# Optimization experiments

Hardware: AMD Instinct MI355X
Metric: run time of the kernel (lower is better)

The kernel has to match this reference:

```python
import jax, jax.numpy as jnp
import numpy as np

HEADS = 4
DIM_HEAD = 32
SCALE = DIM_HEAD ** (-0.5)


def setup_inputs() -> dict:
    key = jax.random.key(0)
    k1, k2, k3, k4 = jax.random.split(key, 4)
    dim = 256
    hidden = HEADS * DIM_HEAD  # 128
    x = jax.random.normal(k1, (8, dim, 48, 48), dtype=jnp.float32)
    w_qkv = jax.random.normal(k2, (3 * hidden, dim), dtype=jnp.float32) * (dim ** -0.5)
    w_out = jax.random.normal(k3, (dim, hidden), dtype=jnp.float32) * (hidden ** -0.5)
    b_out = jax.random.normal(k4, (dim,), dtype=jnp.float32) * 0.01
    return {"x": x, "w_qkv": w_qkv, "w_out": w_out, "b_out": b_out}


def reference(x, w_qkv, w_out, b_out):
    b, c, h, w = x.shape
    n = h * w
    xf = x.reshape(b, c, n)                                  # [b, c, n]
    # 1x1 Conv1d (no bias) == pointwise linear over channels
    qkv = jnp.einsum('oc,bcn->bon', w_qkv, xf)               # [b, 3*hidden, n]
    q, k, v = jnp.split(qkv, 3, axis=1)                      # each [b, hidden, n]
    def to_heads(t):
        return t.reshape(b, HEADS, DIM_HEAD, n)              # b h d n
    q, k, v = to_heads(q) * SCALE, to_heads(k), to_heads(v)
    sim = jnp.einsum('bhdi,bhdj->bhij', q, k)                # [b, h, n, n]
    attn = jax.nn.softmax(sim, axis=-1)                      # stable (max-subtracted)
    out = jnp.einsum('bhij,bhdj->bhid', attn, v)             # [b, h, n, d]
    # 'b h (x y) d -> b (h d) x y'
    out = out.transpose(0, 1, 3, 2).reshape(b, HEADS * DIM_HEAD, n)
    y = jnp.einsum('oc,bcn->bon', w_out, out) + b_out[None, :, None]
    return y.reshape(b, c, h, w)
```

## Files before the change

kernel.cpp:

```cpp
#include <hip/hip_runtime.h>
#include <math.h>

#define NB    8
#define CDIM  256
#define NN    2304
#define NH    4
#define DH    32
#define HIDC  128
#define OC3   384
#define SCALE_LOG2E 0.25503524964550864f
#define SEG   2359296
#define LSEG  73728
#define PPARTS 4
#define JCHUNK 576
#define NITER  18

typedef short  bf16x8 __attribute__((ext_vector_type(8)));
typedef float  f32x4  __attribute__((ext_vector_type(4)));

__device__ __forceinline__ unsigned short f2bf(float f) {
    union { float f; unsigned u; } a; a.f = f;
    unsigned r = a.u + 0x7fffu + ((a.u >> 16) & 1u);
    return (unsigned short)(r >> 16);
}

__device__ __forceinline__ unsigned pack_trunc(float lo, float hi) {
    union { float f; unsigned u; } a, b; a.f = lo; b.f = hi;
    return (b.u & 0xFFFF0000u) | (a.u >> 16);
}

__device__ __forceinline__ float bflo(unsigned u) {
    union { unsigned u; float f; } c; c.u = u << 16; return c.f;
}
__device__ __forceinline__ float bfhi(unsigned u) {
    union { unsigned u; float f; } c; c.u = u & 0xFFFF0000u; return c.f;
}

__global__ __launch_bounds__(256) void qkv_proj_kernel(
    const float* __restrict__ x, const float* __restrict__ w,
    unsigned short* __restrict__ qt, unsigned short* __restrict__ kt,
    unsigned short* __restrict__ vtT)
{
    __shared__ unsigned short As[128 * 40];
    __shared__ unsigned short Bs[128 * 40];
    const int Lb   = (int)blockIdx.x;
    const int xcd  = Lb & 7;
    const int t    = Lb >> 3;
    const int sel  = t % 3;
    const int gl   = t / 3;
    const int group = gl * 8 + xcd;
    const int nb   = group % 18;
    const int b    = group / 18;
    const int n0 = nb * 128;
    const int o0 = sel * 128;

    const int tid  = (int)threadIdx.x;
    const int wave = tid >> 6;
    const int lane = tid & 63;
    const int li   = lane & 15;
    const int g    = lane >> 4;
    const int wm = (wave & 1) * 64;
    const int wn = (wave >> 1) * 64;
    const float* xb = x + (size_t)b * CDIM * NN;

    const int aco = (tid & 7) * 4;
    const int aor = tid >> 3;
    const int n4  = (tid & 31) * 4;
    const int c4  = (tid >> 5) * 4;

    f32x4 acc[4][4];
#pragma unroll
    for (int i = 0; i < 4; ++i)
#pragma unroll
        for (int j = 0; j < 4; ++j) acc[i][j] = (f32x4){0.f, 0.f, 0.f, 0.f};

    float4 wv[4], xv[4];
#pragma unroll
    for (int r = 0; r < 4; ++r)
        wv[r] = *(const float4*)&w[(size_t)(o0 + aor + 32 * r) * CDIM + aco];
#pragma unroll
    for (int dd = 0; dd < 4; ++dd)
        xv[dd] = *(const float4*)&xb[(size_t)(c4 + dd) * NN + n0 + n4];

    for (int k0 = 0; k0 < CDIM; k0 += 32) {
        __syncthreads();
#pragma unroll
        for (int r = 0; r < 4; ++r) {
            uint2 pk;
            pk.x = (unsigned)f2bf(wv[r].x) | ((unsigned)f2bf(wv[r].y) << 16);
            pk.y = (unsigned)f2bf(wv[r].z) | ((unsigned)f2bf(wv[r].w) << 16);
            *(uint2*)&As[(aor + 32 * r) * 40 + aco] = pk;
        }
#pragma unroll
        for (int j = 0; j < 4; ++j) {
            uint2 pk;
            pk.x = (unsigned)f2bf(((const float*)&xv[0])[j])
                 | ((unsigned)f2bf(((const float*)&xv[1])[j]) << 16);
            pk.y = (unsigned)f2bf(((const float*)&xv[2])[j])
                 | ((unsigned)f2bf(((const float*)&xv[3])[j]) << 16);
            *(uint2*)&Bs[(n4 + j) * 40 + c4] = pk;
        }
        __syncthreads();

        const int kn = (k0 + 32 < CDIM) ? (k0 + 32) : k0;
#pragma unroll
        for (int r = 0; r < 4; ++r)
            wv[r] = *(const float4*)&w[(size_t)(o0 + aor + 32 * r) * CDIM + kn + aco];
#pragma unroll
        for (int dd = 0; dd < 4; ++dd)
            xv[dd] = *(const float4*)&xb[(size_t)(kn + c4 + dd) * NN + n0 + n4];

        bf16x8 af[4], bfr[4];
#pragma unroll
        for (int mt = 0; mt < 4; ++mt)
            af[mt] = *(const bf16x8*)&As[(wm + mt * 16 + li) * 40 + g * 8];
#pragma unroll
        for (int nt = 0; nt < 4; ++nt)
            bfr[nt] = *(const bf16x8*)&Bs[(wn + nt * 16 + li) * 40 + g * 8];
#pragma unroll
        for (int mt = 0; mt < 4; ++mt)
#pragma unroll
            for (int nt = 0; nt < 4; ++nt)
                acc[mt][nt] = __builtin_amdgcn_mfma_f32_16x16x32_bf16(
                    af[mt], bfr[nt], acc[mt][nt], 0, 0, 0);
    }

    if (sel < 2) {
        unsigned short* dst = (sel == 0) ? qt : kt;
        const float mul = (sel == 0) ? SCALE_LOG2E : 1.0f;
#pragma unroll
        for (int mt = 0; mt < 4; ++mt) {
            const int ob = o0 + wm + mt * 16 + g * 4;
            const int d0 = ob & 31;
            const int h  = (ob & 127) >> 5;
            const size_t bh = (size_t)(b * NH + h);
#pragma unroll
            for (int nt = 0; nt < 4; ++nt) {
                const int n = n0 + wn + nt * 16 + li;
                const f32x4 a = acc[mt][nt];
                uint2 pk;
                pk.x = (unsigned)f2bf(a[0] * mul) | ((unsigned)f2bf(a[1] * mul) << 16);
                pk.y = (unsigned)f2bf(a[2] * mul) | ((unsigned)f2bf(a[3] * mul) << 16);
                *(uint2*)&dst[(bh * NN + n) * DH + d0] = pk;
            }
        }
    } else {
#pragma unroll
        for (int mt = 0; mt < 4; ++mt) {
            const int ob = o0 + wm + mt * 16 + g * 4;
            const int d0 = ob & 31;
            const int h  = (ob & 127) >> 5;
            const size_t bh = (size_t)(b * NH + h);
#pragma unroll
            for (int nt = 0; nt < 4; ++nt) {
                const int n = n0 + wn + nt * 16 + li;
                const f32x4 a = acc[mt][nt];
#pragma unroll
                for (int r = 0; r < 4; ++r)
                    vtT[(bh * DH + d0 + r) * (size_t)NN + n] = f2bf(a[r]);
            }
        }
    }
}

__global__ __launch_bounds__(256) void attn_kernel(
    const unsigned short* __restrict__ qt, const unsigned short* __restrict__ kt,
    const unsigned short* __restrict__ vtT, unsigned short* __restrict__ Op,
    float* __restrict__ Lp)
{
    __shared__ unsigned short Pl[4][4][16 * 32];
    const int Lb  = (int)blockIdx.x;
    const int xcd = Lb & 7;
    const int t   = Lb >> 3;
    const int ib  = t % 9;
    const int grp = (t / 9) * 8 + xcd;
    const int bh  = grp >> 2;
    const int part = grp & 3;
    const int jbeg = part * JCHUNK;

    const int tid  = (int)threadIdx.x;
    const int wave = tid >> 6;
    const int lane = tid & 63;
    const int li   = lane & 15;
    const int g    = lane >> 4;
    const int i0   = ib * 256 + wave * 64;

    const unsigned short* qb = qt  + (size_t)bh * NN * DH;
    const unsigned short* kb = kt  + (size_t)bh * NN * DH;
    const unsigned short* vb = vtT + (size_t)bh * DH * NN;

    bf16x8 qfA = *(const bf16x8*)(qb + (size_t)(i0 + li) * DH + g * 8);
    bf16x8 qfB = *(const bf16x8*)(qb + (size_t)(i0 + 16 + li) * DH + g * 8);
    bf16x8 qfC = *(const bf16x8*)(qb + (size_t)(i0 + 32 + li) * DH + g * 8);
    bf16x8 qfD = *(const bf16x8*)(qb + (size_t)(i0 + 48 + li) * DH + g * 8);

    bf16x8 ones;
#pragma unroll
    for (int r = 0; r < 8; ++r) ones[r] = (short)0x3F80;

    f32x4 O0A = {0.f,0.f,0.f,0.f}, O1A = {0.f,0.f,0.f,0.f}, LsA = {0.f,0.f,0.f,0.f};
    f32x4 O0B = {0.f,0.f,0.f,0.f}, O1B = {0.f,0.f,0.f,0.f}, LsB = {0.f,0.f,0.f,0.f};
    f32x4 O0C = {0.f,0.f,0.f,0.f}, O1C = {0.f,0.f,0.f,0.f}, LsC = {0.f,0.f,0.f,0.f};
    f32x4 O0D = {0.f,0.f,0.f,0.f}, O1D = {0.f,0.f,0.f,0.f}, LsD = {0.f,0.f,0.f,0.f};

    unsigned short* plA = &Pl[wave][0][0];
    unsigned short* plB = &Pl[wave][1][0];
    unsigned short* plC = &Pl[wave][2][0];
    unsigned short* plD = &Pl[wave][3][0];
    const int sw  = li & 6;
    const int pw  = li * 32;
    const int wr0 = pw + ((g ^ sw) << 2);
    const int wr1 = pw + (((4 + g) ^ sw) << 2);
    const int rdo = pw + (((2 * g) ^ sw) << 2);

    const unsigned short* kp0 = kb + (size_t)(jbeg + li) * DH + g * 8;
    const unsigned short* kp1 = kp0 + 16 * DH;
    const unsigned short* vp0 = vb + (size_t)li * NN + jbeg + g * 8;
    const unsigned short* vp1 = vp0 + 16 * NN;

    bf16x8 kf0 = *(const bf16x8*)kp0;
    bf16x8 kf1 = *(const bf16x8*)kp1;
    bf16x8 vf0 = *(const bf16x8*)vp0;
    bf16x8 vf1 = *(const bf16x8*)vp1;

#pragma unroll 1
    for (int it = 0; it < NITER; ++it) {
        f32x4 z = {0.f, 0.f, 0.f, 0.f};
        f32x4 s0A = __builtin_amdgcn_mfma_f32_16x16x32_bf16(kf0, qfA, z, 0, 0, 0);
        f32x4 s0B = __builtin_amdgcn_mfma_f32_16x16x32_bf16(kf0, qfB, z, 0, 0, 0);
        f32x4 s0C = __builtin_amdgcn_mfma_f32_16x16x32_bf16(kf0, qfC, z, 0, 0, 0);
        f32x4 s0D = __builtin_amdgcn_mfma_f32_16x16x32_bf16(kf0, qfD, z, 0, 0, 0);
        f32x4 s1A = __builtin_amdgcn_mfma_f32_16x16x32_bf16(kf1, qfA, z, 0, 0, 0);
        f32x4 s1B = __builtin_amdgcn_mfma_f32_16x16x32_bf16(kf1, qfB, z, 0, 0, 0);
        f32x4 s1C = __builtin_amdgcn_mfma_f32_16x16x32_bf16(kf1, qfC, z, 0, 0, 0);
        f32x4 s1D = __builtin_amdgcn_mfma_f32_16x16x32_bf16(kf1, qfD, z, 0, 0, 0);

        kp0 += 32 * DH; kp1 += 32 * DH;
        kf0 = *(const bf16x8*)kp0;
        kf1 = *(const bf16x8*)kp1;

        float p0A[4], p1A[4], p0B[4], p1B[4];
        float p0C[4], p1C[4], p0D[4], p1D[4];
#pragma unroll
        for (int r = 0; r < 4; ++r) {
            p0A[r] = __builtin_amdgcn_exp2f(s0A[r]);
            p1A[r] = __builtin_amdgcn_exp2f(s1A[r]);
            p0B[r] = __builtin_amdgcn_exp2f(s0B[r]);
            p1B[r] = __builtin_amdgcn_exp2f(s1B[r]);
            p0C[r] = __builtin_amdgcn_exp2f(s0C[r]);
            p1C[r] = __builtin_amdgcn_exp2f(s1C[r]);
            p0D[r] = __builtin_amdgcn_exp2f(s0D[r]);
            p1D[r] = __builtin_amdgcn_exp2f(s1D[r]);
        }

        uint2 wa, wb;
        wa.x = pack_trunc(p0A[0], p0A[1]);  wa.y = pack_trunc(p0A[2], p0A[3]);
        wb.x = pack_trunc(p1A[0], p1A[1]);  wb.y = pack_trunc(p1A[2], p1A[3]);
        *(uint2*)&plA[wr0] = wa;
        *(uint2*)&plA[wr1] = wb;
        wa.x = pack_trunc(p0B[0], p0B[1]);  wa.y = pack_trunc(p0B[2], p0B[3]);
        wb.x = pack_trunc(p1B[0], p1B[1]);  wb.y = pack_trunc(p1B[2], p1B[3]);
        *(uint2*)&plB[wr0] = wa;
        *(uint2*)&plB[wr1] = wb;
        wa.x = pack_trunc(p0C[0], p0C[1]);  wa.y = pack_trunc(p0C[2], p0C[3]);
        wb.x = pack_trunc(p1C[0], p1C[1]);  wb.y = pack_trunc(p1C[2], p1C[3]);
        *(uint2*)&plC[wr0] = wa;
        *(uint2*)&plC[wr1] = wb;
        wa.x = pack_trunc(p0D[0], p0D[1]);  wa.y = pack_trunc(p0D[2], p0D[3]);
        wb.x = pack_trunc(p1D[0], p1D[1]);  wb.y = pack_trunc(p1D[2], p1D[3]);
        *(uint2*)&plD[wr0] = wa;
        *(uint2*)&plD[wr1] = wb;

        bf16x8 pfA = *(const bf16x8*)&plA[rdo];
        bf16x8 pfB = *(const bf16x8*)&plB[rdo];
        bf16x8 pfC = *(const bf16x8*)&plC[rdo];
        bf16x8 pfD = *(const bf16x8*)&plD[rdo];

        O0A = __builtin_amdgcn_mfma_f32_16x16x32_bf16(vf0,  pfA, O0A, 0, 0, 0);
        O0B = __builtin_amdgcn_mfma_f32_16x16x32_bf16(vf0,  pfB, O0B, 0, 0, 0);
        O0C = __builtin_amdgcn_mfma_f32_16x16x32_bf16(vf0,  pfC, O0C, 0, 0, 0);
        O0D = __builtin_amdgcn_mfma_f32_16x16x32_bf16(vf0,  pfD, O0D, 0, 0, 0);
        O1A = __builtin_amdgcn_mfma_f32_16x16x32_bf16(vf1,  pfA, O1A, 0, 0, 0);
        O1B = __builtin_amdgcn_mfma_f32_16x16x32_bf16(vf1,  pfB, O1B, 0, 0, 0);
        O1C = __builtin_amdgcn_mfma_f32_16x16x32_bf16(vf1,  pfC, O1C, 0, 0, 0);
        O1D = __builtin_amdgcn_mfma_f32_16x16x32_bf16(vf1,  pfD, O1D, 0, 0, 0);
        LsA = __builtin_amdgcn_mfma_f32_16x16x32_bf16(ones, pfA, LsA, 0, 0, 0);
        LsB = __builtin_amdgcn_mfma_f32_16x16x32_bf16(ones, pfB, LsB, 0, 0, 0);
        LsC = __builtin_amdgcn_mfma_f32_16x16x32_bf16(ones, pfC, LsC, 0, 0, 0);
        LsD = __builtin_amdgcn_mfma_f32_16x16x32_bf16(ones, pfD, LsD, 0, 0, 0);

        vp0 += 32; vp1 += 32;
        vf0 = *(const bf16x8*)vp0;
        vf1 = *(const bf16x8*)vp1;
    }

    unsigned short* obA = Op + (size_t)part * SEG + (size_t)bh * DH * NN + i0 + li;
    unsigned short* obB = obA + 16;
    unsigned short* obC = obA + 32;
    unsigned short* obD = obA + 48;
#pragma unroll
    for (int r = 0; r < 4; ++r) {
        obA[(size_t)(4 * g + r)      * NN] = f2bf(O0A[r]);
        obA[(size_t)(16 + 4 * g + r) * NN] = f2bf(O1A[r]);
        obB[(size_t)(4 * g + r)      * NN] = f2bf(O0B[r]);
        obB[(size_t)(16 + 4 * g + r) * NN] = f2bf(O1B[r]);
        obC[(size_t)(4 * g + r)      * NN] = f2bf(O0C[r]);
        obC[(size_t)(16 + 4 * g + r) * NN] = f2bf(O1C[r]);
        obD[(size_t)(4 * g + r)      * NN] = f2bf(O0D[r]);
        obD[(size_t)(16 + 4 * g + r) * NN] = f2bf(O1D[r]);
    }
    if (g == 0) {
        float* lpb = Lp + (size_t)part * LSEG + (size_t)bh * NN + i0 + li;
        lpb[0]  = LsA[0];
        lpb[16] = LsB[0];
        lpb[32] = LsC[0];
        lpb[48] = LsD[0];
    }
}

__global__ __launch_bounds__(256) void out_proj_kernel(
    const unsigned short* __restrict__ Op, const float* __restrict__ Lp,
    const float* __restrict__ w, const float* __restrict__ bias,
    float* __restrict__ y)
{
    __shared__ unsigned short As[128 * 40];
    __shared__ unsigned short Bs[128 * 40];
    __shared__ float Linv[4][128];
    const int Lb   = (int)blockIdx.x;
    const int xcd  = Lb & 7;
    const int t    = Lb >> 3;
    const int so_  = t % 2;
    const int gl   = t / 2;
    const int group = gl * 8 + xcd;
    const int nb   = group % 18;
    const int b    = group / 18;
    const int n0 = nb * 128;
    const int o0 = so_ * 128;

    const int tid  = (int)threadIdx.x;
    const int wave = tid >> 6;
    const int lane = tid & 63;
    const int li   = lane & 15;
    const int g    = lane >> 4;
    const int wm = (wave & 1) * 64;
    const int wn = (wave >> 1) * 64;

    const int aco = (tid & 7) * 4;
    const int aor = tid >> 3;
    const int n4  = (tid & 31) * 4;
    const int d4  = (tid >> 5) * 4;

    {
        const int h = tid >> 6, nb2 = tid & 63;
#pragma unroll
        for (int half = 0; half < 2; ++half) {
            const int n = nb2 + 64 * half;
            float s = 0.f;
#pragma unroll
            for (int p = 0; p < PPARTS; ++p)
                s += Lp[(size_t)p * LSEG + (size_t)(b * NH + h) * NN + n0 + n];
            Linv[h][n] = 1.0f / s;
        }
    }

    f32x4 acc[4][4];
#pragma unroll
    for (int i = 0; i < 4; ++i)
#pragma unroll
        for (int j = 0; j < 4; ++j) acc[i][j] = (f32x4){0.f, 0.f, 0.f, 0.f};

    float4 wv[4];
    uint2  ov[PPARTS][4];
#pragma unroll
    for (int r = 0; r < 4; ++r)
        wv[r] = *(const float4*)&w[(size_t)(o0 + aor + 32 * r) * HIDC + aco];
    {
        const size_t bh0 = (size_t)(b * NH);
#pragma unroll
        for (int p = 0; p < PPARTS; ++p)
#pragma unroll
            for (int dd = 0; dd < 4; ++dd)
                ov[p][dd] = *(const uint2*)&Op[(size_t)p * SEG
                              + (bh0 * DH + d4 + dd) * (size_t)NN + n0 + n4];
    }

    for (int k0 = 0; k0 < HIDC; k0 += 32) {
        __syncthreads();
#pragma unroll
        for (int r = 0; r < 4; ++r) {
            uint2 pk;
            pk.x = (unsigned)f2bf(wv[r].x) | ((unsigned)f2bf(wv[r].y) << 16);
            pk.y = (unsigned)f2bf(wv[r].z) | ((unsigned)f2bf(wv[r].w) << 16);
            *(uint2*)&As[(aor + 32 * r) * 40 + aco] = pk;
        }
        const int h = k0 >> 5;
        {
            float s[4][4];
#pragma unroll
            for (int dd = 0; dd < 4; ++dd)
#pragma unroll
                for (int j = 0; j < 4; ++j) s[dd][j] = 0.f;
#pragma unroll
            for (int p = 0; p < PPARTS; ++p) {
#pragma unroll
                for (int dd = 0; dd < 4; ++dd) {
                    const uint2 u = ov[p][dd];
                    s[dd][0] += bflo(u.x); s[dd][1] += bfhi(u.x);
                    s[dd][2] += bflo(u.y); s[dd][3] += bfhi(u.y);
                }
            }
#pragma unroll
            for (int j = 0; j < 4; ++j) {
                const float lv = Linv[h][n4 + j];
                uint2 pk;
                pk.x = (unsigned)f2bf(s[0][j] * lv) | ((unsigned)f2bf(s[1][j] * lv) << 16);
                pk.y = (unsigned)f2bf(s[2][j] * lv) | ((unsigned)f2bf(s[3][j] * lv) << 16);
                *(uint2*)&Bs[(n4 + j) * 40 + d4] = pk;
            }
        }
        __syncthreads();

        const int kn = (k0 + 32 < HIDC) ? (k0 + 32) : k0;
        const size_t bhn = (size_t)(b * NH + (kn >> 5));
#pragma unroll
        for (int r = 0; r < 4; ++r)
            wv[r] = *(const float4*)&w[(size_t)(o0 + aor + 32 * r) * HIDC + kn + aco];
#pragma unroll
        for (int p = 0; p < PPARTS; ++p)
#pragma unroll
            for (int dd = 0; dd < 4; ++dd)
                ov[p][dd] = *(const uint2*)&Op[(size_t)p * SEG
                              + (bhn * DH + d4 + dd) * (size_t)NN + n0 + n4];

        bf16x8 af[4], bfr[4];
#pragma unroll
        for (int mt = 0; mt < 4; ++mt)
            af[mt] = *(const bf16x8*)&As[(wm + mt * 16 + li) * 40 + g * 8];
#pragma unroll
        for (int nt = 0; nt < 4; ++nt)
            bfr[nt] = *(const bf16x8*)&Bs[(wn + nt * 16 + li) * 40 + g * 8];
#pragma unroll
        for (int mt = 0; mt < 4; ++mt)
#pragma unroll
            for (int nt = 0; nt < 4; ++nt)
                acc[mt][nt] = __builtin_amdgcn_mfma_f32_16x16x32_bf16(
                    af[mt], bfr[nt], acc[mt][nt], 0, 0, 0);
    }

#pragma unroll
    for (int mt = 0; mt < 4; ++mt) {
        const int ob = o0 + wm + mt * 16 + g * 4;
        const float b0 = bias[ob], b1 = bias[ob + 1], b2 = bias[ob + 2], b3 = bias[ob + 3];
#pragma unroll
        for (int nt = 0; nt < 4; ++nt) {
            const int n = n0 + wn + nt * 16 + li;
            const f32x4 a = acc[mt][nt];
            float* yb = y + ((size_t)(b * CDIM + ob)) * NN + n;
            yb[0]              = a[0] + b0;
            yb[(size_t)NN]     = a[1] + b1;
            yb[(size_t)2 * NN] = a[2] + b2;
            yb[(size_t)3 * NN] = a[3] + b3;
        }
    }
}

extern "C" void kernel_launch(void* const* d_in, const int* in_sizes, int n_in,
                              void* d_out, int out_size, void* d_ws, size_t ws_size,
                              hipStream_t stream)
{
    (void)in_sizes; (void)n_in; (void)out_size; (void)ws_size;
    const float* x     = (const float*)d_in[0];
    const float* w_qkv = (const float*)d_in[1];
    const float* w_out = (const float*)d_in[2];
    const float* b_out = (const float*)d_in[3];
    float* y = (float*)d_out;

    unsigned short* qt  = (unsigned short*)d_ws;
    unsigned short* kt  = qt + SEG;
    unsigned short* vtT = kt + SEG;
    unsigned short* Op  = vtT + SEG;
    float* Lp = (float*)(Op + (size_t)PPARTS * SEG);

    qkv_proj_kernel<<<dim3(432), 256, 0, stream>>>(x, w_qkv, qt, kt, vtT);

    attn_kernel<<<dim3(1152), 256, 0, stream>>>(qt, kt, vtT, Op, Lp);

    out_proj_kernel<<<dim3(288), 256, 0, stream>>>(Op, Lp, w_out, b_out, y);
}
```

Baseline: 142.0 us.

## Pre-transpose inputs to bf16 and drop LDS staging in projection GEMMs

Adds a prep kernel that converts x to a bf16 [b, n, c] layout and w_qkv to bf16, so the QKV projection loads MFMA fragments straight from global memory with register double-buffering instead of staging through LDS with barriers. The attention kernel now writes its partial outputs in a [bh, n, d] layout with packed vector stores. The output projection reads those rows directly as fragments, summing the parts and normalizing in registers without LDS tiles. The cost is an extra kernel launch plus a full round trip of x through memory, and the projections lose LDS reuse, so each wave issues more global loads. The converted inputs are kept in scratch space that the attention kernel overwrites later.

Result: slower. 161.7 us (+13.9%).

```diff
diff --git a/kernel.cpp b/kernel.cpp
--- a/kernel.cpp
+++ b/kernel.cpp
@@ -17,6 +17,7 @@
 
 typedef short  bf16x8 __attribute__((ext_vector_type(8)));
 typedef float  f32x4  __attribute__((ext_vector_type(4)));
+typedef unsigned u32x4 __attribute__((ext_vector_type(4)));
 
 __device__ __forceinline__ unsigned short f2bf(float f) {
     union { float f; unsigned u; } a; a.f = f;
@@ -36,13 +37,51 @@
     union { unsigned u; float f; } c; c.u = u & 0xFFFF0000u; return c.f;
 }
 
+__global__ __launch_bounds__(256) void prep_kernel(
+    const float* __restrict__ x, const float* __restrict__ w_qkv,
+    unsigned short* __restrict__ xT, unsigned short* __restrict__ wq)
+{
+    const int blk = (int)blockIdx.x;
+    const int tid = (int)threadIdx.x;
+    if (blk < 1152) {
+        const int b  = blk / 144;
+        const int r  = blk % 144;
+        const int n0 = (r % 36) * 64;
+        const int c0 = (r / 36) * 64;
+        const int n  = n0 + (tid & 63);
+        const int cc = c0 + (tid >> 6) * 16;
+        const float* xb = x + (size_t)b * CDIM * NN;
+        float v[16];
+#pragma unroll
+        for (int e = 0; e < 16; ++e)
+            v[e] = xb[(size_t)(cc + e) * NN + n];
+        unsigned pk[8];
+#pragma unroll
+        for (int e = 0; e < 8; ++e)
+            pk[e] = (unsigned)f2bf(v[2 * e]) | ((unsigned)f2bf(v[2 * e + 1]) << 16);
+        unsigned short* dst = xT + ((size_t)b * NN + n) * CDIM + cc;
+        *(u32x4*)(dst)     = *(u32x4*)&pk[0];
+        *(u32x4*)(dst + 8) = *(u32x4*)&pk[4];
+    } else {
+        const int base = ((blk - 1152) * 256 + tid) * 16;
+        float v[16];
+#pragma unroll
+        for (int e = 0; e < 4; ++e)
+            *(float4*)&v[4 * e] = *(const float4*)&w_qkv[base + 4 * e];
+        unsigned pk[8];
+#pragma unroll
+        for (int e = 0; e < 8; ++e)
+            pk[e] = (unsigned)f2bf(v[2 * e]) | ((unsigned)f2bf(v[2 * e + 1]) << 16);
+        *(u32x4*)&wq[base]     = *(u32x4*)&pk[0];
+        *(u32x4*)&wq[base + 8] = *(u32x4*)&pk[4];
+    }
+}
+
 __global__ __launch_bounds__(256) void qkv_proj_kernel(
-    const float* __restrict__ x, const float* __restrict__ w,
+    const unsigned short* __restrict__ wq, const unsigned short* __restrict__ xT,
     unsigned short* __restrict__ qt, unsigned short* __restrict__ kt,
     unsigned short* __restrict__ vtT)
 {
-    __shared__ unsigned short As[128 * 40];
-    __shared__ unsigned short Bs[128 * 40];
     const int Lb   = (int)blockIdx.x;
     const int xcd  = Lb & 7;
     const int t    = Lb >> 3;
@@ -61,12 +100,7 @@
     const int g    = lane >> 4;
     const int wm = (wave & 1) * 64;
     const int wn = (wave >> 1) * 64;
-    const float* xb = x + (size_t)b * CDIM * NN;
-
-    const int aco = (tid & 7) * 4;
-    const int aor = tid >> 3;
-    const int n4  = (tid & 31) * 4;
-    const int c4  = (tid >> 5) * 4;
+    const unsigned short* xb = xT + (size_t)b * NN * CDIM;
 
     f32x4 acc[4][4];
 #pragma unroll
@@ -74,55 +108,36 @@
 #pragma unroll
         for (int j = 0; j < 4; ++j) acc[i][j] = (f32x4){0.f, 0.f, 0.f, 0.f};
 
-    float4 wv[4], xv[4];
-#pragma unroll
-    for (int r = 0; r < 4; ++r)
-        wv[r] = *(const float4*)&w[(size_t)(o0 + aor + 32 * r) * CDIM + aco];
-#pragma unroll
-    for (int dd = 0; dd < 4; ++dd)
-        xv[dd] = *(const float4*)&xb[(size_t)(c4 + dd) * NN + n0 + n4];
-
+    const unsigned short* awp[4];
+    const unsigned short* bxp[4];
+    bf16x8 af[4], bfr[4], afn[4], bfn[4];
+#pragma unroll
+    for (int mt = 0; mt < 4; ++mt) {
+        awp[mt] = wq + (size_t)(o0 + wm + mt * 16 + li) * CDIM + g * 8;
+        af[mt]  = *(const bf16x8*)awp[mt];
+    }
+#pragma unroll
+    for (int nt = 0; nt < 4; ++nt) {
+        bxp[nt] = xb + (size_t)(n0 + wn + nt * 16 + li) * CDIM + g * 8;
+        bfr[nt] = *(const bf16x8*)bxp[nt];
+    }
+
+#pragma unroll 2
     for (int k0 = 0; k0 < CDIM; k0 += 32) {
-        __syncthreads();
-#pragma unroll
-        for (int r = 0; r < 4; ++r) {
-            uint2 pk;
-            pk.x = (unsigned)f2bf(wv[r].x) | ((unsigned)f2bf(wv[r].y) << 16);
-            pk.y = (unsigned)f2bf(wv[r].z) | ((unsigned)f2bf(wv[r].w) << 16);
-            *(uint2*)&As[(aor + 32 * r) * 40 + aco] = pk;
-        }
-#pragma unroll
-        for (int j = 0; j < 4; ++j) {
-            uint2 pk;
-            pk.x = (unsigned)f2bf(((const float*)&xv[0])[j])
-                 | ((unsigned)f2bf(((const float*)&xv[1])[j]) << 16);
-            pk.y = (unsigned)f2bf(((const float*)&xv[2])[j])
-                 | ((unsigned)f2bf(((const float*)&xv[3])[j]) << 16);
-            *(uint2*)&Bs[(n4 + j) * 40 + c4] = pk;
-        }
-        __syncthreads();
-
-        const int kn = (k0 + 32 < CDIM) ? (k0 + 32) : k0;
-#pragma unroll
-        for (int r = 0; r < 4; ++r)
-            wv[r] = *(const float4*)&w[(size_t)(o0 + aor + 32 * r) * CDIM + kn + aco];
-#pragma unroll
-        for (int dd = 0; dd < 4; ++dd)
-            xv[dd] = *(const float4*)&xb[(size_t)(kn + c4 + dd) * NN + n0 + n4];
-
-        bf16x8 af[4], bfr[4];
-#pragma unroll
-        for (int mt = 0; mt < 4; ++mt)
-            af[mt] = *(const bf16x8*)&As[(wm + mt * 16 + li) * 40 + g * 8];
-#pragma unroll
-        for (int nt = 0; nt < 4; ++nt)
-            bfr[nt] = *(const bf16x8*)&Bs[(wn + nt * 16 + li) * 40 + g * 8];
+#pragma unroll
+        for (int mt = 0; mt < 4; ++mt) { awp[mt] += 32; afn[mt] = *(const bf16x8*)awp[mt]; }
+#pragma unroll
+        for (int nt = 0; nt < 4; ++nt) { bxp[nt] += 32; bfn[nt] = *(const bf16x8*)bxp[nt]; }
 #pragma unroll
         for (int mt = 0; mt < 4; ++mt)
 #pragma unroll
             for (int nt = 0; nt < 4; ++nt)
                 acc[mt][nt] = __builtin_amdgcn_mfma_f32_16x16x32_bf16(
                     af[mt], bfr[nt], acc[mt][nt], 0, 0, 0);
+#pragma unroll
+        for (int mt = 0; mt < 4; ++mt) af[mt] = afn[mt];
+#pragma unroll
+        for (int nt = 0; nt < 4; ++nt) bfr[nt] = bfn[nt];
     }
 
     if (sel < 2) {
@@ -294,21 +309,36 @@
         vf1 = *(const bf16x8*)vp1;
     }
 
-    unsigned short* obA = Op + (size_t)part * SEG + (size_t)bh * DH * NN + i0 + li;
-    unsigned short* obB = obA + 16;
-    unsigned short* obC = obA + 32;
-    unsigned short* obD = obA + 48;
-#pragma unroll
-    for (int r = 0; r < 4; ++r) {
-        obA[(size_t)(4 * g + r)      * NN] = f2bf(O0A[r]);
-        obA[(size_t)(16 + 4 * g + r) * NN] = f2bf(O1A[r]);
-        obB[(size_t)(4 * g + r)      * NN] = f2bf(O0B[r]);
-        obB[(size_t)(16 + 4 * g + r) * NN] = f2bf(O1B[r]);
-        obC[(size_t)(4 * g + r)      * NN] = f2bf(O0C[r]);
-        obC[(size_t)(16 + 4 * g + r) * NN] = f2bf(O1C[r]);
-        obD[(size_t)(4 * g + r)      * NN] = f2bf(O0D[r]);
-        obD[(size_t)(16 + 4 * g + r) * NN] = f2bf(O1D[r]);
-    }
+    unsigned short* obA = Op + (size_t)part * SEG + ((size_t)bh * NN + i0 + li) * DH;
+    unsigned short* obB = obA + (size_t)16 * DH;
+    unsigned short* obC = obA + (size_t)32 * DH;
+    unsigned short* obD = obA + (size_t)48 * DH;
+    uint2 st;
+    st.x = (unsigned)f2bf(O0A[0]) | ((unsigned)f2bf(O0A[1]) << 16);
+    st.y = (unsigned)f2bf(O0A[2]) | ((unsigned)f2bf(O0A[3]) << 16);
+    *(uint2*)&obA[4 * g] = st;
+    st.x = (unsigned)f2bf(O1A[0]) | ((unsigned)f2bf(O1A[1]) << 16);
+    st.y = (unsigned)f2bf(O1A[2]) | ((unsigned)f2bf(O1A[3]) << 16);
+    *(uint2*)&obA[16 + 4 * g] = st;
+    st.x = (unsigned)f2bf(O0B[0]) | ((unsigned)f2bf(O0B[1]) << 16);
+    st.y = (unsigned)f2bf(O0B[2]) | ((unsigned)f2bf(O0B[3]) << 16);
+    *(uint2*)&obB[4 * g] = st;
+    st.x = (unsigned)f2bf(O1B[0]) | ((unsigned)f2bf(O1B[1]) << 16);
+    st.y = (unsigned)f2bf(O1B[2]) | ((unsigned)f2bf(O1B[3]) << 16);
+    *(uint2*)&obB[16 + 4 * g] = st;
+    st.x = (unsigned)f2bf(O0C[0]) | ((unsigned)f2bf(O0C[1]) << 16);
+    st.y = (unsigned)f2bf(O0C[2]) | ((unsigned)f2bf(O0C[3]) << 16);
+    *(uint2*)&obC[4 * g] = st;
+    st.x = (unsigned)f2bf(O1C[0]) | ((unsigned)f2bf(O1C[1]) << 16);
+    st.y = (unsigned)f2bf(O1C[2]) | ((unsigned)f2bf(O1C[3]) << 16);
+    *(uint2*)&obC[16 + 4 * g] = st;
+    st.x = (unsigned)f2bf(O0D[0]) | ((unsigned)f2bf(O0D[1]) << 16);
+    st.y = (unsigned)f2bf(O0D[2]) | ((unsigned)f2bf(O0D[3]) << 16);
+    *(uint2*)&obD[4 * g] = st;
+    st.x = (unsigned)f2bf(O1D[0]) | ((unsigned)f2bf(O1D[1]) << 16);
+    st.y = (unsigned)f2bf(O1D[2]) | ((unsigned)f2bf(O1D[3]) << 16);
+    *(uint2*)&obD[16 + 4 * g] = st;
+
     if (g == 0) {
         float* lpb = Lp + (size_t)part * LSEG + (size_t)bh * NN + i0 + li;
         lpb[0]  = LsA[0];
@@ -323,8 +353,6 @@
     const float* __restrict__ w, const float* __restrict__ bias,
     float* __restrict__ y)
 {
-    __shared__ unsigned short As[128 * 40];
-    __shared__ unsigned short Bs[128 * 40];
     __shared__ float Linv[4][128];
     const int Lb   = (int)blockIdx.x;
     const int xcd  = Lb & 7;
@@ -345,11 +373,6 @@
     const int wm = (wave & 1) * 64;
     const int wn = (wave >> 1) * 64;
 
-    const int aco = (tid & 7) * 4;
-    const int aor = tid >> 3;
-    const int n4  = (tid & 31) * 4;
-    const int d4  = (tid >> 5) * 4;
-
     {
         const int h = tid >> 6, nb2 = tid & 63;
 #pragma unroll
@@ -362,6 +385,7 @@
             Linv[h][n] = 1.0f / s;
         }
     }
+    __syncthreads();
 
     f32x4 acc[4][4];
 #pragma unroll
@@ -369,82 +393,44 @@
 #pragma unroll
         for (int j = 0; j < 4; ++j) acc[i][j] = (f32x4){0.f, 0.f, 0.f, 0.f};
 
-    float4 wv[4];
-    uint2  ov[PPARTS][4];
-#pragma unroll
-    for (int r = 0; r < 4; ++r)
-        wv[r] = *(const float4*)&w[(size_t)(o0 + aor + 32 * r) * HIDC + aco];
-    {
-        const size_t bh0 = (size_t)(b * NH);
-#pragma unroll
-        for (int p = 0; p < PPARTS; ++p)
-#pragma unroll
-            for (int dd = 0; dd < 4; ++dd)
-                ov[p][dd] = *(const uint2*)&Op[(size_t)p * SEG
-                              + (bh0 * DH + d4 + dd) * (size_t)NN + n0 + n4];
-    }
-
-    for (int k0 = 0; k0 < HIDC; k0 += 32) {
-        __syncthreads();
-#pragma unroll
-        for (int r = 0; r < 4; ++r) {
-            uint2 pk;
-            pk.x = (unsigned)f2bf(wv[r].x) | ((unsigned)f2bf(wv[r].y) << 16);
-            pk.y = (unsigned)f2bf(wv[r].z) | ((unsigned)f2bf(wv[r].w) << 16);
-            *(uint2*)&As[(aor + 32 * r) * 40 + aco] = pk;
-        }
-        const int h = k0 >> 5;
-        {
-            float s[4][4];
-#pragma unroll
-            for (int dd = 0; dd < 4; ++dd)
-#pragma unroll
-                for (int j = 0; j < 4; ++j) s[dd][j] = 0.f;
-#pragma unroll
-            for (int p = 0; p < PPARTS; ++p) {
-#pragma unroll
-                for (int dd = 0; dd < 4; ++dd) {
-                    const uint2 u = ov[p][dd];
-                    s[dd][0] += bflo(u.x); s[dd][1] += bfhi(u.x);
-                    s[dd][2] += bflo(u.y); s[dd][3] += bfhi(u.y);
-                }
+#pragma unroll
+    for (int h = 0; h < 4; ++h) {
+        const int k0 = h * 32;
+        bf16x8 af[4];
+#pragma unroll
+        for (int mt = 0; mt < 4; ++mt) {
+            const float* wr = w + (size_t)(o0 + wm + mt * 16 + li) * HIDC + k0 + g * 8;
+            const float4 wa = *(const float4*)wr;
+            const float4 wb2 = *(const float4*)(wr + 4);
+            u32x4 q;
+            q[0] = (unsigned)f2bf(wa.x)  | ((unsigned)f2bf(wa.y)  << 16);
+            q[1] = (unsigned)f2bf(wa.z)  | ((unsigned)f2bf(wa.w)  << 16);
+            q[2] = (unsigned)f2bf(wb2.x) | ((unsigned)f2bf(wb2.y) << 16);
+            q[3] = (unsigned)f2bf(wb2.z) | ((unsigned)f2bf(wb2.w) << 16);
+            af[mt] = __builtin_bit_cast(bf16x8, q);
+        }
+        const size_t rowb = ((size_t)(b * NH + h) * NN + n0);
+#pragma unroll
+        for (int nt = 0; nt < 4; ++nt) {
+            const int n = wn + nt * 16 + li;
+            u32x4 u0 = *(const u32x4*)&Op[(size_t)0 * SEG + (rowb + n) * DH + g * 8];
+            u32x4 u1 = *(const u32x4*)&Op[(size_t)1 * SEG + (rowb + n) * DH + g * 8];
+            u32x4 u2 = *(const u32x4*)&Op[(size_t)2 * SEG + (rowb + n) * DH + g * 8];
+            u32x4 u3 = *(const u32x4*)&Op[(size_t)3 * SEG + (rowb + n) * DH + g * 8];
+            const float lv = Linv[h][n];
+            u32x4 pk;
+#pragma unroll
+            for (int e = 0; e < 4; ++e) {
+                const float s0 = bflo(u0[e]) + bflo(u1[e]) + bflo(u2[e]) + bflo(u3[e]);
+                const float s1 = bfhi(u0[e]) + bfhi(u1[e]) + bfhi(u2[e]) + bfhi(u3[e]);
+                pk[e] = (unsigned)f2bf(s0 * lv) | ((unsigned)f2bf(s1 * lv) << 16);
             }
-#pragma unroll
-            for (int j = 0; j < 4; ++j) {
-                const float lv = Linv[h][n4 + j];
-                uint2 pk;
-                pk.x = (unsigned)f2bf(s[0][j] * lv) | ((unsigned)f2bf(s[1][j] * lv) << 16);
-                pk.y = (unsigned)f2bf(s[2][j] * lv) | ((unsigned)f2bf(s[3][j] * lv) << 16);
-                *(uint2*)&Bs[(n4 + j) * 40 + d4] = pk;
-            }
-        }
-        __syncthreads();
-
-        const int kn = (k0 + 32 < HIDC) ? (k0 + 32) : k0;
-        const size_t bhn = (size_t)(b * NH + (kn >> 5));
-#pragma unroll
-        for (int r = 0; r < 4; ++r)
-            wv[r] = *(const float4*)&w[(size_t)(o0 + aor + 32 * r) * HIDC + kn + aco];
-#pragma unroll
-        for (int p = 0; p < PPARTS; ++p)
-#pragma unroll
-            for (int dd = 0; dd < 4; ++dd)
-                ov[p][dd] = *(const uint2*)&Op[(size_t)p * SEG
-                              + (bhn * DH + d4 + dd) * (size_t)NN + n0 + n4];
-
-        bf16x8 af[4], bfr[4];
-#pragma unroll
-        for (int mt = 0; mt < 4; ++mt)
-            af[mt] = *(const bf16x8*)&As[(wm + mt * 16 + li) * 40 + g * 8];
-#pragma unroll
-        for (int nt = 0; nt < 4; ++nt)
-            bfr[nt] = *(const bf16x8*)&Bs[(wn + nt * 16 + li) * 40 + g * 8];
-#pragma unroll
-        for (int mt = 0; mt < 4; ++mt)
-#pragma unroll
-            for (int nt = 0; nt < 4; ++nt)
+            const bf16x8 bfr = __builtin_bit_cast(bf16x8, pk);
+#pragma unroll
+            for (int mt = 0; mt < 4; ++mt)
                 acc[mt][nt] = __builtin_amdgcn_mfma_f32_16x16x32_bf16(
-                    af[mt], bfr[nt], acc[mt][nt], 0, 0, 0);
+                    af[mt], bfr, acc[mt][nt], 0, 0, 0);
+        }
     }
 
 #pragma unroll
@@ -481,7 +467,12 @@
     unsigned short* Op  = vtT + SEG;
     float* Lp = (float*)(Op + (size_t)PPARTS * SEG);
 
-    qkv_proj_kernel<<<dim3(432), 256, 0, stream>>>(x, w_qkv, qt, kt, vtT);
+    unsigned short* xT = Op;
+    unsigned short* wq = Op + (size_t)2 * SEG;
+
+    prep_kernel<<<dim3(1176), 256, 0, stream>>>(x, w_qkv, xT, wq);
+
+    qkv_proj_kernel<<<dim3(432), 256, 0, stream>>>(wq, xT, qt, kt, vtT);
 
     attn_kernel<<<dim3(1152), 256, 0, stream>>>(qt, kt, vtT, Op, Lp);
 
```
